# Kernel tuning notes

Hardware: AMD Instinct MI355X
Metric: run time of the kernel (lower is better)

The kernel has to match this reference:

```python
import jax, jax.numpy as jnp
import numpy as np

B, L, H, R = 4, 192, 768, 24


def setup_inputs() -> dict:
    key = jax.random.key(0)
    ks = jax.random.split(key, 18)
    s = 0.02
    inp = {
        "embed_tokens": jax.random.normal(ks[0], (B, L, H), dtype=jnp.float32),
        "attention_mask": jnp.ones((B, L), dtype=jnp.int32),
        "target_rel": jax.random.randint(ks[1], (B,), 0, R),
        # hidden_relational: Linear(H, H//2) stored as [in, out]
        "W_relh": jax.random.normal(ks[2], (H, H // 2), dtype=jnp.float32) * s,
        "b_relh": jnp.zeros((H // 2,), dtype=jnp.float32),
        # rel_judge: Linear(H//2, R)
        "W_rj": jax.random.normal(ks[3], (H // 2, R), dtype=jnp.float32) * s,
        "b_rj": jnp.zeros((R,), dtype=jnp.float32),
        # hidden_corres: Linear(2H, H)
        "W_corr": jax.random.normal(ks[4], (2 * H, H), dtype=jnp.float32) * s,
        "b_corr": jnp.zeros((H,), dtype=jnp.float32),
        # global_corr: Linear(H, 1)
        "W_gc": jax.random.normal(ks[5], (H, 1), dtype=jnp.float32) * s,
        "b_gc": jnp.zeros((1,), dtype=jnp.float32),
        # rel_embedding: Embedding(R, H)
        "rel_emb": jax.random.normal(ks[6], (R, H), dtype=jnp.float32) * s,
        # hidden_tag: Linear(2H, H) (fusion_type='concat' => multiplier 2)
        "W_tag": jax.random.normal(ks[7], (2 * H, H), dtype=jnp.float32) * s,
        "b_tag": jnp.zeros((H,), dtype=jnp.float32),
        # tag_subject / tag_object: Linear(H, 3)
        "W_sub": jax.random.normal(ks[8], (H, 3), dtype=jnp.float32) * s,
        "b_sub": jnp.zeros((3,), dtype=jnp.float32),
        "W_obj": jax.random.normal(ks[9], (H, 3), dtype=jnp.float32) * s,
        "b_obj": jnp.zeros((3,), dtype=jnp.float32),
    }
    return inp


def reference(embed_tokens, attention_mask, target_rel,
              W_relh, b_relh, W_rj, b_rj,
              W_corr, b_corr, W_gc, b_gc,
              rel_emb, W_tag, b_tag,
              W_sub, b_sub, W_obj, b_obj):
    # mode == 'train' path of PRGC.forward, with embed_tokens standing in for
    # bert(...)['last_hidden_state'].
    mask = attention_mask.astype(embed_tokens.dtype)  # [B,L]
    # stage 1: masked average pool -> relation judgement
    avg = jnp.sum(embed_tokens * mask[:, :, None], axis=1) / jnp.sum(mask, axis=1)[:, None]  # [B,H]
    rel_hidden = jax.nn.relu(avg @ W_relh + b_relh)
    stage1 = rel_hidden @ W_rj + b_rj  # [B,R]

    # correspondence matrix. concat_matrix[b,i,j] = [embed[b,j], embed[b,i]]
    # Linear on a concat is separable: split W_corr into the halves acting on
    # each operand, compute two [B,L,H] projections, sum with broadcasting.
    Hd = W_corr.shape[0] // 2
    h_first = embed_tokens @ W_corr[:Hd]   # acts on embed[b,j]
    h_second = embed_tokens @ W_corr[Hd:]  # acts on embed[b,i]
    corres_hidden = jax.nn.relu(h_first[:, None, :, :] + h_second[:, :, None, :] + b_corr)  # [B,L,L,H]
    pred_corres = corres_hidden @ W_gc + b_gc  # [B,L,L,1]

    # stage 2 tagging (train mode: gather gold relation embeddings)
    rel_e = rel_emb[target_rel]  # [B,H]
    rel_e = jnp.broadcast_to(rel_e[:, None, :], embed_tokens.shape)  # [B,L,H]
    fusion = jnp.concatenate([rel_e, embed_tokens], axis=-1) @ W_tag + b_tag  # [B,L,H] (no activation, as in source)
    subj_pred_tag = fusion @ W_sub + b_sub  # [B,L,3]
    obj_pred_tag = fusion @ W_obj + b_obj   # [B,L,3]
    return (stage1, subj_pred_tag, obj_pred_tag, pred_corres)
```

## Files before the change

kernel.cpp:

```cpp
#include <hip/hip_runtime.h>

#define H   768
#define Hh  384
#define LL  192
#define RR  24
#define HH  589824

typedef __attribute__((ext_vector_type(8))) short bf16x8;
typedef __attribute__((ext_vector_type(4))) float f32x4;

__device__ __forceinline__ unsigned short f2bf(float f) {
    unsigned int u = __float_as_uint(f);
    return (unsigned short)((u + 0x7FFF + ((u >> 16) & 1)) >> 16);
}

__device__ __forceinline__ void gload16(const void* g, void* l) {
    __builtin_amdgcn_global_load_lds(
        (const __attribute__((address_space(1))) unsigned int*)g,
        (__attribute__((address_space(3))) unsigned int*)l, 16, 0, 0);
}

__device__ __forceinline__ float wred(float v) {
#pragma unroll
    for (int off = 1; off < 64; off <<= 1) v += __shfl_xor(v, off);
    return v;
}

__global__ __launch_bounds__(256) void k_pre(
    const float* __restrict__ emb, const int* __restrict__ mask,
    const float* __restrict__ W_corr, const float* __restrict__ W_tag,
    const float* __restrict__ W_gc, const float* __restrict__ b_corr,
    const float* __restrict__ W_sub, const float* __restrict__ b_sub,
    const float* __restrict__ W_obj, const float* __restrict__ b_obj,
    const float* __restrict__ b_tag,
    float* __restrict__ avg_ws, unsigned short* __restrict__ embh,
    unsigned short* __restrict__ wct0, unsigned short* __restrict__ wct1,
    float* __restrict__ W8_ws, float* __restrict__ V8_ws,
    float* __restrict__ cb_ws, float* __restrict__ bc_ws)
{
    const int bid = blockIdx.x, tid = threadIdx.x;

    if (bid < 24) {
        __shared__ float msk[LL];
        __shared__ float part[32];
        __shared__ float msumS;
        __shared__ float4 red4[8][32];
        const int b  = bid / 6;
        const int h0 = (bid % 6) * 128;
        const int tx = tid & 31, ty = tid >> 5;
        if (tid < LL) msk[tid] = (float)mask[b * LL + tid];
        __syncthreads();
        if (tid < 32) {
            float s = 0.f;
            for (int k = tid; k < LL; k += 32) s += msk[k];
            part[tid] = s;
        }
        __syncthreads();
        if (tid == 0) {
            float s = 0.f;
            for (int k = 0; k < 32; ++k) s += part[k];
            msumS = s;
        }
        float4 acc = make_float4(0.f, 0.f, 0.f, 0.f);
        for (int l = ty; l < LL; l += 8) {
            const float m = msk[l];
            const float4 v = *(const float4*)(emb + (size_t)(b * LL + l) * H + h0 + tx * 4);
            acc.x += v.x * m; acc.y += v.y * m; acc.z += v.z * m; acc.w += v.w * m;
        }
        red4[ty][tx] = acc;
        __syncthreads();
        if (tid < 32) {
            float4 s = red4[0][tid];
#pragma unroll
            for (int r = 1; r < 8; ++r) {
                s.x += red4[r][tid].x; s.y += red4[r][tid].y;
                s.z += red4[r][tid].z; s.w += red4[r][tid].w;
            }
            const float inv = 1.f / msumS;
            s.x *= inv; s.y *= inv; s.z *= inv; s.w *= inv;
            *(float4*)(avg_ws + (size_t)b * H + h0 + tid * 4) = s;
        }
        return;
    }

    if (bid < 168) {
        const size_t t = (size_t)(bid - 24) * 256 + tid;
        const float* s = emb + t * 16;
        union { unsigned short u[16]; uint4 v[2]; } pk;
#pragma unroll
        for (int q = 0; q < 4; ++q) {
            const float4 v = *(const float4*)(s + q * 4);
            pk.u[q * 4 + 0] = f2bf(v.x); pk.u[q * 4 + 1] = f2bf(v.y);
            pk.u[q * 4 + 2] = f2bf(v.z); pk.u[q * 4 + 3] = f2bf(v.w);
        }
        *(uint4*)(embh + t * 16)     = pk.v[0];
        *(uint4*)(embh + t * 16 + 8) = pk.v[1];
        return;
    }

    if (bid < 744) {
        const int local = bid - 168;
        const int m  = local / 288;
        const int r2 = local % 288;
        const int ko = r2 / 3, nb = r2 % 3;
        const int n  = nb * 256 + tid;
        const float* src = (m == 0) ? W_corr : W_corr + HH;
        unsigned short* dst = (m == 0) ? wct0 : wct1;
        union { unsigned short u[8]; uint4 v; } pk;
#pragma unroll
        for (int q = 0; q < 8; ++q)
            pk.u[q] = f2bf(src[(size_t)(ko * 8 + q) * H + n]);
        *(uint4*)(dst + (size_t)n * H + ko * 8) = pk.v;
        return;
    }

    if (bid < 936) {
        const int wave = tid >> 6, lane = tid & 63;
        const int k = (bid - 744) * 4 + wave;
        const float* rc0 = W_corr + (size_t)k * H;
        const float* rc1 = W_corr + (size_t)(HH) + (size_t)k * H;
        const float* rtl = W_tag + (size_t)k * H;
        const float* rth = W_tag + (size_t)(H + k) * H;
        float u0 = 0.f, u1 = 0.f;
        float wsv[3] = {0, 0, 0}, wov[3] = {0, 0, 0};
        float vsv[3] = {0, 0, 0}, vov[3] = {0, 0, 0};
#pragma unroll
        for (int it = 0; it < 3; ++it) {
            const int h = lane * 4 + it * 256;
            const float4 c0 = *(const float4*)(rc0 + h);
            const float4 c1 = *(const float4*)(rc1 + h);
            const float4 tl = *(const float4*)(rtl + h);
            const float4 th = *(const float4*)(rth + h);
            const float4 g  = *(const float4*)(W_gc + h);
            float su[12], ob[12];
            *(float4*)&su[0] = *(const float4*)(W_sub + h * 3);
            *(float4*)&su[4] = *(const float4*)(W_sub + h * 3 + 4);
            *(float4*)&su[8] = *(const float4*)(W_sub + h * 3 + 8);
            *(float4*)&ob[0] = *(const float4*)(W_obj + h * 3);
            *(float4*)&ob[4] = *(const float4*)(W_obj + h * 3 + 4);
            *(float4*)&ob[8] = *(const float4*)(W_obj + h * 3 + 8);
            u0 += c0.x * g.x + c0.y * g.y + c0.z * g.z + c0.w * g.w;
            u1 += c1.x * g.x + c1.y * g.y + c1.z * g.z + c1.w * g.w;
            const float t4[4] = {th.x, th.y, th.z, th.w};
            const float l4[4] = {tl.x, tl.y, tl.z, tl.w};
#pragma unroll
            for (int d = 0; d < 4; ++d)
#pragma unroll
                for (int c = 0; c < 3; ++c) {
                    wsv[c] += t4[d] * su[d * 3 + c];
                    vsv[c] += l4[d] * su[d * 3 + c];
                    wov[c] += t4[d] * ob[d * 3 + c];
                    vov[c] += l4[d] * ob[d * 3 + c];
                }
        }
        u0 = wred(u0); u1 = wred(u1);
#pragma unroll
        for (int c = 0; c < 3; ++c) {
            wsv[c] = wred(wsv[c]); wov[c] = wred(wov[c]);
            vsv[c] = wred(vsv[c]); vov[c] = wred(vov[c]);
        }
        if (lane == 0) {
            *(float4*)(W8_ws + k * 8)     = make_float4(u0, u1, wsv[0], wsv[1]);
            *(float4*)(W8_ws + k * 8 + 4) = make_float4(wsv[2], wov[0], wov[1], wov[2]);
            *(float4*)(V8_ws + k * 8)     = make_float4(vsv[0], vsv[1], vsv[2], vov[0]);
            *(float4*)(V8_ws + k * 8 + 4) = make_float4(vov[1], vov[2], 0.f, 0.f);
        }
        return;
    }

    {
        const int wave = tid >> 6, lane = tid & 63;
        if (wave == 0) {
            float cs[3] = {0, 0, 0}, co[3] = {0, 0, 0};
#pragma unroll
            for (int it = 0; it < 3; ++it) {
                const int h = lane * 4 + it * 256;
                const float4 bt = *(const float4*)(b_tag + h);
                float su[12], ob[12];
                *(float4*)&su[0] = *(const float4*)(W_sub + h * 3);
                *(float4*)&su[4] = *(const float4*)(W_sub + h * 3 + 4);
                *(float4*)&su[8] = *(const float4*)(W_sub + h * 3 + 8);
                *(float4*)&ob[0] = *(const float4*)(W_obj + h * 3);
                *(float4*)&ob[4] = *(const float4*)(W_obj + h * 3 + 4);
                *(float4*)&ob[8] = *(const float4*)(W_obj + h * 3 + 8);
                const float b4[4] = {bt.x, bt.y, bt.z, bt.w};
#pragma unroll
                for (int d = 0; d < 4; ++d)
#pragma unroll
                    for (int c = 0; c < 3; ++c) {
                        cs[c] += b4[d] * su[d * 3 + c];
                        co[c] += b4[d] * ob[d * 3 + c];
                    }
            }
#pragma unroll
            for (int c = 0; c < 3; ++c) { cs[c] = wred(cs[c]); co[c] = wred(co[c]); }
            if (lane == 0) {
#pragma unroll
                for (int c = 0; c < 3; ++c) {
                    cb_ws[c]     = cs[c] + b_sub[c];
                    cb_ws[3 + c] = co[c] + b_obj[c];
                }
            }
        } else if (wave == 1) {
            float s = 0.f;
#pragma unroll
            for (int it = 0; it < 3; ++it) {
                const int h = lane * 4 + it * 256;
                const float4 bcv = *(const float4*)(b_corr + h);
                const float4 g   = *(const float4*)(W_gc + h);
                s += bcv.x * g.x + bcv.y * g.y + bcv.z * g.z + bcv.w * g.w;
            }
            s = wred(s);
            if (lane == 0) bc_ws[0] = s;
        }
    }
}

__global__ __launch_bounds__(256) void k_main(
    const unsigned short* __restrict__ embh, const unsigned short* __restrict__ wct0,
    const unsigned short* __restrict__ wct1, const float* __restrict__ b_corr,
    const float* __restrict__ W_relh, const float* __restrict__ avg_ws,
    const int* __restrict__ target_rel, const float* __restrict__ rel_emb,
    const float* __restrict__ V8_ws, const float* __restrict__ cb_ws,
    float* __restrict__ hfb, float* __restrict__ hsb,
    float* __restrict__ relh_part, float* __restrict__ tb_ws)
{
    __shared__ unsigned short As[2][4096];
    __shared__ unsigned short Bs[2][4096];
    const int bid = blockIdx.x, tid = threadIdx.x;

    if (bid >= 288) {
        if (bid < 480) {
            float* red = (float*)&As[0][0];
            const int rb = bid - 288;
            const int kc = rb & 7;
            const int t2 = rb >> 3;
            const int b  = t2 / 6;
            const int o0 = (t2 % 6) * 64;
            const int tx = tid & 63, ty = tid >> 6;
            const int h0 = kc * 96 + ty * 24;
            float s = 0.f;
            for (int h = h0; h < h0 + 24; ++h)
                s += avg_ws[(size_t)b * H + h] * W_relh[(size_t)h * Hh + o0 + tx];
            red[ty * 64 + tx] = s;
            __syncthreads();
            if (ty == 0)
                relh_part[(size_t)(kc * 4 + b) * Hh + o0 + tx] =
                    red[tx] + red[64 + tx] + red[128 + tx] + red[192 + tx];
        } else {
            const int b = tid >> 6, lane = tid & 63;
            const float* re = rel_emb + (size_t)target_rel[b] * H;
            float t[6] = {0, 0, 0, 0, 0, 0};
#pragma unroll
            for (int it = 0; it < 12; ++it) {
                const int k = lane + it * 64;
                const float rl = re[k];
                const float4 a = *(const float4*)(V8_ws + k * 8);
                const float4 v = *(const float4*)(V8_ws + k * 8 + 4);
                t[0] += rl * a.x; t[1] += rl * a.y; t[2] += rl * a.z;
                t[3] += rl * a.w; t[4] += rl * v.x; t[5] += rl * v.y;
            }
#pragma unroll
            for (int c = 0; c < 6; ++c) t[c] = wred(t[c]);
            if (lane == 0) {
#pragma unroll
                for (int c = 0; c < 6; ++c)
                    tb_ws[b * 8 + c] = t[c] + cb_ws[c];
            }
        }
        return;
    }

    const int sel = bid / 144;
    const int tt  = bid % 144;
    const int mt = tt % 12, nt = tt / 12;
    const int m0 = mt * 64, n0 = nt * 64;
    const unsigned short* Bsrc = sel ? wct1 : wct0;
    float* C = sel ? hsb : hfb;

    const int wv = tid >> 6, ln = tid & 63;
    const int lr = ln & 15, ko = ln >> 4;
    const int wr = (wv >> 1) * 32, wc = (wv & 1) * 32;

    f32x4 acc[2][2];
#pragma unroll
    for (int mi = 0; mi < 2; ++mi)
#pragma unroll
        for (int ni = 0; ni < 2; ++ni)
            acc[mi][ni] = (f32x4){0.f, 0.f, 0.f, 0.f};

    auto stage = [&](int buf, int k0) {
#pragma unroll
        for (int it = 0; it < 2; ++it) {
            const int sbase = it * 256 + wv * 64;
            const int slot = sbase + ln;
            const int r = slot >> 3, c = slot & 7;
            const int cs = c ^ (r & 7);
            gload16(embh + (size_t)(m0 + r) * H + k0 + cs * 8, &As[buf][sbase * 8]);
            gload16(Bsrc + (size_t)(n0 + r) * H + k0 + cs * 8, &Bs[buf][sbase * 8]);
        }
    };

    stage(0, 0);
    int cur = 0;
    for (int ks = 0; ks < 12; ++ks) {
        __syncthreads();
        if (ks < 11) stage(cur ^ 1, (ks + 1) * 64);
        bf16x8 af[2][2], bfr[2][2];
#pragma unroll
        for (int mi = 0; mi < 2; ++mi) {
            const int r = wr + mi * 16 + lr;
#pragma unroll
            for (int kc = 0; kc < 2; ++kc) {
                const int qs = (kc * 4 + ko) ^ (r & 7);
                af[kc][mi] = *(const bf16x8*)(&As[cur][r * 64 + qs * 8]);
            }
        }
#pragma unroll
        for (int ni = 0; ni < 2; ++ni) {
            const int r = wc + ni * 16 + lr;
#pragma unroll
            for (int kc = 0; kc < 2; ++kc) {
                const int qs = (kc * 4 + ko) ^ (r & 7);
                bfr[kc][ni] = *(const bf16x8*)(&Bs[cur][r * 64 + qs * 8]);
            }
        }
#pragma unroll
        for (int kc = 0; kc < 2; ++kc)
#pragma unroll
            for (int mi = 0; mi < 2; ++mi)
#pragma unroll
                for (int ni = 0; ni < 2; ++ni)
                    acc[mi][ni] = __builtin_amdgcn_mfma_f32_16x16x32_bf16(
                        af[kc][mi], bfr[kc][ni], acc[mi][ni], 0, 0, 0);
        cur ^= 1;
    }

    float cb[2];
#pragma unroll
    for (int ni = 0; ni < 2; ++ni)
        cb[ni] = (sel == 0) ? b_corr[n0 + wc + ni * 16 + lr] : 0.f;
#pragma unroll
    for (int mi = 0; mi < 2; ++mi)
#pragma unroll
        for (int ni = 0; ni < 2; ++ni) {
            const int m = m0 + wr + mi * 16 + ko * 4;
            const int n = n0 + wc + ni * 16 + lr;
#pragma unroll
            for (int rr = 0; rr < 4; ++rr)
                C[(size_t)(m + rr) * H + n] = acc[mi][ni][rr] + cb[ni];
        }
}

__global__ __launch_bounds__(256) void k_tail(
    const float* __restrict__ hfb, const float* __restrict__ hsb,
    const float* __restrict__ emb, const float* __restrict__ W8_ws,
    const float* __restrict__ tb_ws, const float* __restrict__ relh_part,
    const float* __restrict__ b_relh, const float* __restrict__ W_gc,
    const float* __restrict__ W_rj, const float* __restrict__ b_rj,
    float* __restrict__ cpart, float* __restrict__ hfw_ws,
    float* __restrict__ out)
{
    __shared__ float hfT[96][34];
    const int bid = blockIdx.x, tid = threadIdx.x;

    if (bid < 576) {
        const int s    = bid & 7;
        const int tile = bid >> 3;
        const int b   = tile / 18;
        const int rem = tile % 18;
        const int i0  = (rem / 6) * 64;
        const int j0  = (rem % 6) * 32;
        const int h0  = s * 96;
        const int tx = tid & 15, ty = tid >> 4;

#pragma unroll
        for (int it = 0; it < 3; ++it) {
            const int j = tid >> 3, q = tid & 7;
            const int k = it * 32 + q * 4;
            const float4 fv = *(const float4*)(hfb + (size_t)(b * LL + j0 + j) * H + h0 + k);
            hfT[k + 0][j] = fv.x;
            hfT[k + 1][j] = fv.y;
            hfT[k + 2][j] = fv.z;
            hfT[k + 3][j] = fv.w;
        }
        __syncthreads();

        float acc[4][2] = {{0.f}};
        float hsr[4][8];
        const float* hsbase = hsb + (size_t)(b * LL + i0 + ty * 4) * H + h0;

        for (int kb = 0; kb < 96; kb += 8) {
#pragma unroll
            for (int ii = 0; ii < 4; ++ii) {
                const float4 v0 = *(const float4*)(hsbase + (size_t)ii * H + kb);
                const float4 v1 = *(const float4*)(hsbase + (size_t)ii * H + kb + 4);
                hsr[ii][0] = v0.x; hsr[ii][1] = v0.y; hsr[ii][2] = v0.z; hsr[ii][3] = v0.w;
                hsr[ii][4] = v1.x; hsr[ii][5] = v1.y; hsr[ii][6] = v1.z; hsr[ii][7] = v1.w;
            }
            const float4 wa = *(const float4*)(W_gc + h0 + kb);
            const float4 wb = *(const float4*)(W_gc + h0 + kb + 4);
            const float wreg[8] = {wa.x, wa.y, wa.z, wa.w, wb.x, wb.y, wb.z, wb.w};
#pragma unroll
            for (int k8 = 0; k8 < 8; ++k8) {
                const int kk = kb + k8;
                const float2 f2 = *(const float2*)&hfT[kk][tx * 2];
                const float w = wreg[k8];
#pragma unroll
                for (int ii = 0; ii < 4; ++ii) {
                    acc[ii][0] += fabsf(f2.x + hsr[ii][k8]) * w;
                    acc[ii][1] += fabsf(f2.y + hsr[ii][k8]) * w;
                }
            }
        }
#pragma unroll
        for (int ii = 0; ii < 4; ++ii) {
            *(float2*)(cpart + (size_t)s * 147456 + (size_t)b * 36864
                       + (size_t)(i0 + ty * 4 + ii) * LL + j0 + tx * 2) =
                make_float2(acc[ii][0], acc[ii][1]);
        }
    } else if (bid < 768) {
        const int wave = tid >> 6, lane = tid & 63;
        const int r = (bid - 576) * 4 + wave;
        const int b = r / LL;
        const float* er = emb + (size_t)r * H;
        float s0 = 0.f, s1 = 0.f;
        float t[6] = {0, 0, 0, 0, 0, 0};
#pragma unroll
        for (int it = 0; it < 12; ++it) {
            const int h = lane + it * 64;
            const float e = er[h];
            const float4 a = *(const float4*)(W8_ws + h * 8);
            const float4 v = *(const float4*)(W8_ws + h * 8 + 4);
            s0 += e * a.x; s1 += e * a.y;
            t[0] += e * a.z; t[1] += e * a.w; t[2] += e * v.x;
            t[3] += e * v.y; t[4] += e * v.z; t[5] += e * v.w;
        }
        s0 = wred(s0); s1 = wred(s1);
#pragma unroll
        for (int c = 0; c < 6; ++c) t[c] = wred(t[c]);
        if (lane == 0) {
            hfw_ws[r] = s0;
            hfw_ws[768 + r] = s1;
#pragma unroll
            for (int c = 0; c < 3; ++c) {
                out[96 + r * 3 + c]   = t[c]     + tb_ws[b * 8 + c];
                out[2400 + r * 3 + c] = t[3 + c] + tb_ws[b * 8 + 3 + c];
            }
        }
    } else {
        float* relhS = &hfT[0][0];
        for (int i = tid; i < 4 * Hh; i += 256) {
            const int b = i / Hh, o = i % Hh;
            float s = b_relh[o];
#pragma unroll
            for (int kc = 0; kc < 8; ++kc)
                s += relh_part[(size_t)(kc * 4 + b) * Hh + o];
            relhS[i] = fmaxf(s, 0.f);
        }
        __syncthreads();
        if (tid < 96) {
            const int b = tid / RR, rj = tid % RR;
            float s = b_rj[rj];
            for (int k = 0; k < Hh; ++k)
                s += relhS[b * Hh + k] * W_rj[k * RR + rj];
            out[b * RR + rj] = s;
        }
    }
}

__global__ __launch_bounds__(256) void k_merge(
    const float* __restrict__ cpart, const float* __restrict__ hfw_ws,
    const float* __restrict__ bc_ws, const float* __restrict__ b_gc,
    float* __restrict__ out)
{
    const int idx = blockIdx.x * 256 + threadIdx.x;
    const int b  = idx / 9216;
    const int rr = idx % 9216;
    const int i  = rr / 48;
    const int j4 = (rr % 48) * 4;
    const size_t off = (size_t)b * 36864 + (size_t)i * LL + j4;

    float4 p = make_float4(0.f, 0.f, 0.f, 0.f);
#pragma unroll
    for (int s = 0; s < 8; ++s) {
        const float4 v = *(const float4*)(cpart + (size_t)s * 147456 + off);
        p.x += v.x; p.y += v.y; p.z += v.z; p.w += v.w;
    }
    const float4 hw = *(const float4*)(hfw_ws + b * LL + j4);
    const float hs = hfw_ws[768 + b * LL + i];
    const float bc = bc_ws[0];
    const float bg = b_gc[0];

    float4 o;
    o.x = 0.5f * (p.x + hw.x + hs + bc) + bg;
    o.y = 0.5f * (p.y + hw.y + hs + bc) + bg;
    o.z = 0.5f * (p.z + hw.z + hs + bc) + bg;
    o.w = 0.5f * (p.w + hw.w + hs + bc) + bg;
    *(float4*)(out + 4704 + off) = o;
}

extern "C" void kernel_launch(void* const* d_in, const int* in_sizes, int n_in,
                              void* d_out, int out_size, void* d_ws, size_t ws_size,
                              hipStream_t stream) {
    const float* emb    = (const float*)d_in[0];
    const int*   mask   = (const int*)d_in[1];
    const int*   trel   = (const int*)d_in[2];
    const float* W_relh = (const float*)d_in[3];
    const float* b_relh = (const float*)d_in[4];
    const float* W_rj   = (const float*)d_in[5];
    const float* b_rj   = (const float*)d_in[6];
    const float* W_corr = (const float*)d_in[7];
    const float* b_corr = (const float*)d_in[8];
    const float* W_gc   = (const float*)d_in[9];
    const float* b_gc   = (const float*)d_in[10];
    const float* relemb = (const float*)d_in[11];
    const float* W_tag  = (const float*)d_in[12];
    const float* b_tag  = (const float*)d_in[13];
    const float* W_sub  = (const float*)d_in[14];
    const float* b_sub  = (const float*)d_in[15];
    const float* W_obj  = (const float*)d_in[16];
    const float* b_obj  = (const float*)d_in[17];

    float* out = (float*)d_out;
    float* ws  = (float*)d_ws;
    float* hfb  = ws;
    float* hsb  = ws + (size_t)HH;
    unsigned short* embh = (unsigned short*)(ws + (size_t)2 * HH);
    unsigned short* wct0 = embh + (size_t)HH;
    unsigned short* wct1 = wct0 + (size_t)HH;
    float* smalls    = ws + (size_t)2 * HH + (size_t)3 * HH / 2;
    float* avg_ws    = smalls;
    float* W8_ws     = avg_ws + 4 * H;
    float* V8_ws     = W8_ws + 8 * H;
    float* relh_part = V8_ws + 8 * H;
    float* hfw_ws    = relh_part + 32 * Hh;
    float* tb_ws     = hfw_ws + 1536;
    float* cb_ws     = tb_ws + 32;
    float* bc_ws     = cb_ws + 8;
    float* cpart     = bc_ws + 8;

    k_pre<<<937, 256, 0, stream>>>(emb, mask, W_corr, W_tag, W_gc, b_corr,
                                   W_sub, b_sub, W_obj, b_obj, b_tag,
                                   avg_ws, embh, wct0, wct1,
                                   W8_ws, V8_ws, cb_ws, bc_ws);
    k_main<<<481, 256, 0, stream>>>(embh, wct0, wct1, b_corr,
                                    W_relh, avg_ws, trel, relemb,
                                    V8_ws, cb_ws,
                                    hfb, hsb, relh_part, tb_ws);
    k_tail<<<769, 256, 0, stream>>>(hfb, hsb, emb, W8_ws, tb_ws, relh_part,
                                    b_relh, W_gc, W_rj, b_rj,
                                    cpart, hfw_ws, out);
    k_merge<<<144, 256, 0, stream>>>(cpart, hfw_ws, bc_ws, b_gc, out);
}
```

Measured before the change: 51.51 us.

## Split-K the projection GEMM into two halves summed in the tail kernel

The bf16 MFMA projection GEMM in k_main now splits K=768 into two halves of 384, doubling its blocks from 288 to 576 so more of the machine's compute units are busy. Each half writes its own fp32 partial buffer, and k_tail adds the two partials when loading hf and hs. This trades extra workspace, extra global writes, and double the reads in the tail kernel for better GPU occupancy in the GEMM.

Measured after the change: 60.37 us. 17.2% more time.

```diff
diff --git a/kernel.cpp b/kernel.cpp
--- a/kernel.cpp
+++ b/kernel.cpp
@@ -118,7 +118,7 @@
         const int wave = tid >> 6, lane = tid & 63;
         const int k = (bid - 744) * 4 + wave;
         const float* rc0 = W_corr + (size_t)k * H;
-        const float* rc1 = W_corr + (size_t)(HH) + (size_t)k * H;
+        const float* rc1 = W_corr + (size_t)HH + (size_t)k * H;
         const float* rtl = W_tag + (size_t)k * H;
         const float* rth = W_tag + (size_t)(H + k) * H;
         float u0 = 0.f, u1 = 0.f;
@@ -222,17 +222,18 @@
     const float* __restrict__ W_relh, const float* __restrict__ avg_ws,
     const int* __restrict__ target_rel, const float* __restrict__ rel_emb,
     const float* __restrict__ V8_ws, const float* __restrict__ cb_ws,
-    float* __restrict__ hfb, float* __restrict__ hsb,
+    float* __restrict__ hf0, float* __restrict__ hf1,
+    float* __restrict__ hs0, float* __restrict__ hs1,
     float* __restrict__ relh_part, float* __restrict__ tb_ws)
 {
     __shared__ unsigned short As[2][4096];
     __shared__ unsigned short Bs[2][4096];
     const int bid = blockIdx.x, tid = threadIdx.x;
 
-    if (bid >= 288) {
-        if (bid < 480) {
+    if (bid >= 576) {
+        if (bid < 768) {
             float* red = (float*)&As[0][0];
-            const int rb = bid - 288;
+            const int rb = bid - 576;
             const int kc = rb & 7;
             const int t2 = rb >> 3;
             const int b  = t2 / 6;
@@ -271,12 +272,15 @@
         return;
     }
 
-    const int sel = bid / 144;
-    const int tt  = bid % 144;
+    const int half = bid & 1;
+    const int t   = bid >> 1;
+    const int sel = t / 144;
+    const int tt  = t % 144;
     const int mt = tt % 12, nt = tt / 12;
     const int m0 = mt * 64, n0 = nt * 64;
+    const int kbase = half * 384;
     const unsigned short* Bsrc = sel ? wct1 : wct0;
-    float* C = sel ? hsb : hfb;
+    float* C = sel ? (half ? hs1 : hs0) : (half ? hf1 : hf0);
 
     const int wv = tid >> 6, ln = tid & 63;
     const int lr = ln & 15, ko = ln >> 4;
@@ -301,11 +305,11 @@
         }
     };
 
-    stage(0, 0);
+    stage(0, kbase);
     int cur = 0;
-    for (int ks = 0; ks < 12; ++ks) {
+    for (int ks = 0; ks < 6; ++ks) {
         __syncthreads();
-        if (ks < 11) stage(cur ^ 1, (ks + 1) * 64);
+        if (ks < 5) stage(cur ^ 1, kbase + (ks + 1) * 64);
         bf16x8 af[2][2], bfr[2][2];
 #pragma unroll
         for (int mi = 0; mi < 2; ++mi) {
@@ -336,10 +340,10 @@
         cur ^= 1;
     }
 
-    float cb[2];
+    float cbv[2];
 #pragma unroll
     for (int ni = 0; ni < 2; ++ni)
-        cb[ni] = (sel == 0) ? b_corr[n0 + wc + ni * 16 + lr] : 0.f;
+        cbv[ni] = (sel == 0 && half == 0) ? b_corr[n0 + wc + ni * 16 + lr] : 0.f;
 #pragma unroll
     for (int mi = 0; mi < 2; ++mi)
 #pragma unroll
@@ -348,12 +352,13 @@
             const int n = n0 + wc + ni * 16 + lr;
 #pragma unroll
             for (int rr = 0; rr < 4; ++rr)
-                C[(size_t)(m + rr) * H + n] = acc[mi][ni][rr] + cb[ni];
+                C[(size_t)(m + rr) * H + n] = acc[mi][ni][rr] + cbv[ni];
         }
 }
 
 __global__ __launch_bounds__(256) void k_tail(
-    const float* __restrict__ hfb, const float* __restrict__ hsb,
+    const float* __restrict__ hf0, const float* __restrict__ hf1,
+    const float* __restrict__ hs0, const float* __restrict__ hs1,
     const float* __restrict__ emb, const float* __restrict__ W8_ws,
     const float* __restrict__ tb_ws, const float* __restrict__ relh_part,
     const float* __restrict__ b_relh, const float* __restrict__ W_gc,
@@ -378,25 +383,31 @@
         for (int it = 0; it < 3; ++it) {
             const int j = tid >> 3, q = tid & 7;
             const int k = it * 32 + q * 4;
-            const float4 fv = *(const float4*)(hfb + (size_t)(b * LL + j0 + j) * H + h0 + k);
-            hfT[k + 0][j] = fv.x;
-            hfT[k + 1][j] = fv.y;
-            hfT[k + 2][j] = fv.z;
-            hfT[k + 3][j] = fv.w;
+            const size_t o = (size_t)(b * LL + j0 + j) * H + h0 + k;
+            const float4 a = *(const float4*)(hf0 + o);
+            const float4 c = *(const float4*)(hf1 + o);
+            hfT[k + 0][j] = a.x + c.x;
+            hfT[k + 1][j] = a.y + c.y;
+            hfT[k + 2][j] = a.z + c.z;
+            hfT[k + 3][j] = a.w + c.w;
         }
         __syncthreads();
 
         float acc[4][2] = {{0.f}};
         float hsr[4][8];
-        const float* hsbase = hsb + (size_t)(b * LL + i0 + ty * 4) * H + h0;
+        const size_t hsoff = (size_t)(b * LL + i0 + ty * 4) * H + h0;
 
         for (int kb = 0; kb < 96; kb += 8) {
 #pragma unroll
             for (int ii = 0; ii < 4; ++ii) {
-                const float4 v0 = *(const float4*)(hsbase + (size_t)ii * H + kb);
-                const float4 v1 = *(const float4*)(hsbase + (size_t)ii * H + kb + 4);
-                hsr[ii][0] = v0.x; hsr[ii][1] = v0.y; hsr[ii][2] = v0.z; hsr[ii][3] = v0.w;
-                hsr[ii][4] = v1.x; hsr[ii][5] = v1.y; hsr[ii][6] = v1.z; hsr[ii][7] = v1.w;
+                const float4 v0 = *(const float4*)(hs0 + hsoff + (size_t)ii * H + kb);
+                const float4 w0 = *(const float4*)(hs1 + hsoff + (size_t)ii * H + kb);
+                const float4 v1 = *(const float4*)(hs0 + hsoff + (size_t)ii * H + kb + 4);
+                const float4 w1 = *(const float4*)(hs1 + hsoff + (size_t)ii * H + kb + 4);
+                hsr[ii][0] = v0.x + w0.x; hsr[ii][1] = v0.y + w0.y;
+                hsr[ii][2] = v0.z + w0.z; hsr[ii][3] = v0.w + w0.w;
+                hsr[ii][4] = v1.x + w1.x; hsr[ii][5] = v1.y + w1.y;
+                hsr[ii][6] = v1.z + w1.z; hsr[ii][7] = v1.w + w1.w;
             }
             const float4 wa = *(const float4*)(W_gc + h0 + kb);
             const float4 wb = *(const float4*)(W_gc + h0 + kb + 4);
@@ -524,12 +535,14 @@
 
     float* out = (float*)d_out;
     float* ws  = (float*)d_ws;
-    float* hfb  = ws;
-    float* hsb  = ws + (size_t)HH;
-    unsigned short* embh = (unsigned short*)(ws + (size_t)2 * HH);
+    float* hf0 = ws;
+    float* hf1 = ws + (size_t)HH;
+    float* hs0 = ws + (size_t)2 * HH;
+    float* hs1 = ws + (size_t)3 * HH;
+    unsigned short* embh = (unsigned short*)(ws + (size_t)4 * HH);
     unsigned short* wct0 = embh + (size_t)HH;
     unsigned short* wct1 = wct0 + (size_t)HH;
-    float* smalls    = ws + (size_t)2 * HH + (size_t)3 * HH / 2;
+    float* smalls    = ws + (size_t)4 * HH + (size_t)3 * HH / 2;
     float* avg_ws    = smalls;
     float* W8_ws     = avg_ws + 4 * H;
     float* V8_ws     = W8_ws + 8 * H;
@@ -538,18 +551,18 @@
     float* tb_ws     = hfw_ws + 1536;
     float* cb_ws     = tb_ws + 32;
     float* bc_ws     = cb_ws + 8;
-    float* cpart     = bc_ws + 8;
+    float* cpart     = bc_ws + 8 + 200;
 
     k_pre<<<937, 256, 0, stream>>>(emb, mask, W_corr, W_tag, W_gc, b_corr,
                                    W_sub, b_sub, W_obj, b_obj, b_tag,
                                    avg_ws, embh, wct0, wct1,
                                    W8_ws, V8_ws, cb_ws, bc_ws);
-    k_main<<<481, 256, 0, stream>>>(embh, wct0, wct1, b_corr,
+    k_main<<<769, 256, 0, stream>>>(embh, wct0, wct1, b_corr,
                                     W_relh, avg_ws, trel, relemb,
                                     V8_ws, cb_ws,
-                                    hfb, hsb, relh_part, tb_ws);
-    k_tail<<<769, 256, 0, stream>>>(hfb, hsb, emb, W8_ws, tb_ws, relh_part,
-                                    b_relh, W_gc, W_rj, b_rj,
+                                    hf0, hf1, hs0, hs1, relh_part, tb_ws);
+    k_tail<<<769, 256, 0, stream>>>(hf0, hf1, hs0, hs1, emb, W8_ws, tb_ws,
+                                    relh_part, b_relh, W_gc, W_rj, b_rj,
                                     cpart, hfw_ws, out);
     k_merge<<<144, 256, 0, stream>>>(cpart, hfw_ws, bc_ws, b_gc, out);
 }
```
